# Performance work log

Measured on AMD Instinct MI355X. Metric: run time of the kernel, lower is better.

## Reference

```python
import jax, jax.numpy as jnp
import numpy as np

COMMA_ID = 1010   # BERT wordpiece id for ','
H, NH, HD = 768, 8, 96
B, S = 64, 512
NSEG = 17         # 16 commas per row -> 17 segments
EPS = 1e-5


def setup_inputs() -> dict:
    key = jax.random.key(0)
    ks = jax.random.split(key, 16)
    text_hs = jax.random.normal(ks[0], (B, S, H), jnp.float32)
    cols_hs = jax.random.normal(ks[1], (B, S, H), jnp.float32)
    ids = jax.random.randint(ks[2], (B, S), 0, 30522)
    ids = jnp.where(ids == COMMA_ID, COMMA_ID + 1, ids)  # avoid accidental commas
    comma_pos = jnp.arange(16, 257, 16)                  # 16 commas per row
    ids = ids.at[:, comma_pos].set(COMMA_ID)
    sc = 0.02
    wq = jax.random.normal(ks[3], (H, H), jnp.float32) * sc
    wk = jax.random.normal(ks[4], (H, H), jnp.float32) * sc
    wv = jax.random.normal(ks[5], (H, H), jnp.float32) * sc
    bq = jnp.zeros((H,), jnp.float32)
    bk = jnp.zeros((H,), jnp.float32)
    bv = jnp.zeros((H,), jnp.float32)
    wo = jax.random.normal(ks[6], (H, H), jnp.float32) * sc
    bo = jnp.zeros((H,), jnp.float32)
    gamma = jnp.ones((H,), jnp.float32)
    beta = jnp.zeros((H,), jnp.float32)
    w_out = jax.random.normal(ks[7], (1, H), jnp.float32) * sc
    b_out = jnp.zeros((1,), jnp.float32)
    return dict(text_hs=text_hs, cols_hs=cols_hs, wq=wq, wk=wk, wv=wv,
                bq=bq, bk=bk, bv=bv, wo=wo, bo=bo, gamma=gamma, beta=beta,
                w_out=w_out, b_out=b_out, columns_input_ids=ids, n_segments=NSEG)


def _forward(text_hs, cols_hs, wq, wk, wv, bq, bk, bv, wo, bo,
             gamma, beta, w_out, b_out, columns_input_ids, n_segments):
    t = text_hs[:, 1:, :]   # drop first token, as in forward()  [B, L, H]
    c = cols_hs[:, 1:, :]
    L = t.shape[1]
    # --- nn.MultiheadAttention(query=cols, key=value=text), batch_first ---
    q = c @ wq.T + bq
    k = t @ wk.T + bk
    v = t @ wv.T + bv
    split = lambda x: x.reshape(x.shape[0], -1, NH, HD).transpose(0, 2, 1, 3)
    scores = jnp.einsum('bhqd,bhkd->bhqk', split(q), split(k)) / np.sqrt(HD).astype(np.float32)
    attn = jax.nn.softmax(scores, axis=-1)
    ctx = jnp.einsum('bhqk,bhkd->bhqd', attn, split(v))
    ctx = ctx.transpose(0, 2, 1, 3).reshape(c.shape[0], L, H)
    attn_out = ctx @ wo.T + bo
    # --- BatchNorm1d over channels (training-mode batch stats) ---
    xt = attn_out.transpose(0, 2, 1)            # [B, H, L]
    mu = xt.mean(axis=(0, 2), keepdims=True)
    var = xt.var(axis=(0, 2), keepdims=True)     # biased, as torch BN normalization
    xn = (xt - mu) / jnp.sqrt(var + EPS) * gamma[None, :, None] + beta[None, :, None]
    cross_out = c + xn.transpose(0, 2, 1)       # residual add
    fv = (cross_out @ w_out.T + b_out).squeeze(-1)   # [B, L] scores per token
    # --- compose_outputs: mean-pool comma-delimited ragged spans ---
    is_comma = columns_input_ids[:, :L] == COMMA_ID
    seg = jnp.cumsum(is_comma.astype(jnp.int32), axis=1) - is_comma.astype(jnp.int32)
    mask = (jnp.arange(L)[None, :] >= 1) & (~is_comma)    # slice_start=1, commas excluded
    oh = ((seg[:, :, None] == jnp.arange(n_segments)[None, None, :])
          & mask[:, :, None]).astype(fv.dtype)            # [B, L, J]
    sums = jnp.einsum('blj,bl->bj', oh, fv)
    cnt = oh.sum(axis=1)
    return sums / jnp.maximum(cnt, 1.0)                   # [B, n_segments]


def reference(text_hs, cols_hs, wq, wk, wv, bq, bk, bv, wo, bo,
              gamma, beta, w_out, b_out, columns_input_ids, n_segments):
    return _forward(text_hs, cols_hs, wq, wk, wv, bq, bk, bv, wo, bo,
                    gamma, beta, w_out, b_out, columns_input_ids, n_segments)
```

## Files before the change

kernel.cpp:

```cpp
#include <hip/hip_runtime.h>
#include <hip/hip_bf16.h>

#define COMMA_IDC 1010
#define NHEAD 8
#define Ll 511
#define Mrows 32704
#define NSEG 17

typedef __attribute__((ext_vector_type(8))) short bf16x8;
typedef __attribute__((ext_vector_type(4))) float f32x4;
typedef unsigned short u16;
typedef unsigned int u32;
typedef unsigned long long u64;

__device__ __forceinline__ u16 f2b(float f) {
  __hip_bfloat16 h = __float2bfloat16(f);
  return *reinterpret_cast<u16*>(&h);
}
__device__ __forceinline__ float b2f(u16 u) {
  u32 x = ((u32)u) << 16;
  return __builtin_bit_cast(float, x);
}

__device__ __forceinline__ void gld_lds16(const void* g, void* l) {
  __builtin_amdgcn_global_load_lds(
      (const __attribute__((address_space(1))) void*)(u64)g,
      (__attribute__((address_space(3))) void*)(u32)(u64)l,
      16, 0, 0);
}

#define MFMA16(a, b, c) __builtin_amdgcn_mfma_f32_16x16x32_bf16(a, b, c, 0, 0, 0)

__global__ void conv_sliced(const float4* __restrict__ src, ushort4* __restrict__ dst) {
  int b = blockIdx.y;
  int idx = blockIdx.x * 256 + threadIdx.x;
  if (idx >= Ll * 192) return;
  int l = idx / 192, c = idx - l * 192;
  float4 v = src[(b * 512 + l + 1) * 192 + c];
  ushort4 o; o.x = f2b(v.x); o.y = f2b(v.y); o.z = f2b(v.z); o.w = f2b(v.w);
  dst[(b * Ll + l) * 192 + c] = o;
}

__global__ void conv_flat(const float4* __restrict__ src, ushort4* __restrict__ dst, int n4) {
  int i = blockIdx.x * 256 + threadIdx.x;
  if (i < n4) {
    float4 v = src[i];
    ushort4 o; o.x = f2b(v.x); o.y = f2b(v.y); o.z = f2b(v.z); o.w = f2b(v.w);
    dst[i] = o;
  }
}

__global__ void zero_kernel(float* p, int n) {
  int i = blockIdx.x * 256 + threadIdx.x;
  if (i < n) p[i] = 0.f;
}

template<int NTILES, int NOUT, int QNT>
__global__ __launch_bounds__(256) void gemmk(
    const u16* __restrict__ A0, const u16* __restrict__ A1, const u16* __restrict__ W,
    const float* __restrict__ b0, const float* __restrict__ b1, const float* __restrict__ b2,
    u16* __restrict__ outp)
{
  __shared__ __align__(16) u16 sMem[16384];
  u16* sA = sMem;
  u16* sW = sMem + 8192;

  const int tid = threadIdx.x;
  const int lane = tid & 63, wid = tid >> 6;
  int fid = blockIdx.x;
  int xcd = fid & 7, t = fid >> 3;
  int mrow = xcd * 32 + t / NTILES;
  int ncol = t - (t / NTILES) * NTILES;
  const int m0 = mrow * 128, n0 = ncol * 128;
  const u16* __restrict__ A = (ncol < QNT) ? A0 : A1;
  const int fr = lane & 15, fq = lane >> 4;
  const int wr = wid >> 1, wc = wid & 1;

  f32x4 acc[4][4] = {};

  const int r0 = tid >> 2, kc0 = tid & 3;
  const u16* gA0 = A + (u64)(m0 + r0) * 768 + kc0 * 8;
  const u16* gA1 = A + (u64)(m0 + r0 + 64) * 768 + kc0 * 8;
  const u16* gW0 = W + (u64)(n0 + r0) * 768 + kc0 * 8;
  const u16* gW1 = W + (u64)(n0 + r0 + 64) * 768 + kc0 * 8;
  u16* lA0 = sA + wid * 512;
  u16* lA1 = sA + 2048 + wid * 512;
  u16* lW0 = sW + wid * 512;
  u16* lW1 = sW + 2048 + wid * 512;

  auto STAGE = [&](int buf, int kofs) {
    gld_lds16(gA0 + kofs, lA0 + buf * 4096);
    gld_lds16(gA1 + kofs, lA1 + buf * 4096);
    gld_lds16(gW0 + kofs, lW0 + buf * 4096);
    gld_lds16(gW1 + kofs, lW1 + buf * 4096);
  };
  auto COMPUTE = [&](int buf) {
    const u16* pa = sA + buf * 4096 + (wr * 64 + fr) * 32 + fq * 8;
    const u16* pb = sW + buf * 4096 + (wc * 64 + fr) * 32 + fq * 8;
    bf16x8 a[4], b[4];
#pragma unroll
    for (int i = 0; i < 4; i++) a[i] = *(const bf16x8*)(pa + i * 16 * 32);
#pragma unroll
    for (int j = 0; j < 4; j++) b[j] = *(const bf16x8*)(pb + j * 16 * 32);
#pragma unroll
    for (int i = 0; i < 4; i++)
#pragma unroll
      for (int j = 0; j < 4; j++)
        acc[i][j] = MFMA16(a[i], b[j], acc[i][j]);
  };

  STAGE(0, 0);
  for (int k0 = 0; k0 < 768; k0 += 64) {
    __syncthreads();
    if (k0 + 32 < 768) STAGE(1, k0 + 32);
    COMPUTE(0);
    __syncthreads();
    if (k0 + 64 < 768) STAGE(0, k0 + 64);
    COMPUTE(1);
  }

  const int seg = n0 / 768, boff = n0 - seg * 768;
  const float* bp = (seg == 0) ? b0 : ((seg == 1) ? b1 : b2);
  float bj[4];
#pragma unroll
  for (int j = 0; j < 4; j++) bj[j] = bp[boff + wc * 64 + j * 16 + fr];

#pragma unroll
  for (int half = 0; half < 2; half++) {
    __syncthreads();
#pragma unroll
    for (int i2 = 0; i2 < 2; i2++) {
      int i = half * 2 + i2;
#pragma unroll
      for (int j = 0; j < 4; j++) {
#pragma unroll
        for (int r = 0; r < 4; r++) {
          int lr = wr * 32 + i2 * 16 + fq * 4 + r;
          sMem[lr * 136 + wc * 64 + j * 16 + fr] = f2b(acc[i][j][r] + bj[j]);
        }
      }
    }
    __syncthreads();
#pragma unroll
    for (int c = 0; c < 4; c++) {
      int cc = tid + c * 256;
      int lr = cc >> 4, ch = cc & 15;
      int m = m0 + (lr >> 5) * 64 + half * 32 + (lr & 31);
      if (m < Mrows)
        *(bf16x8*)(outp + (u64)m * NOUT + n0 + ch * 8) =
            *(const bf16x8*)(sMem + lr * 136 + ch * 8);
    }
  }
}

__global__ __launch_bounds__(256) void vtrans(const u16* __restrict__ QKV, u16* __restrict__ VT) {
  __shared__ __align__(16) u16 sT[128 * 128];
  int bh = blockIdx.y;
  int b = bh >> 3, h = bh & 7;
  int l0 = blockIdx.x * 128;
  u16* outp = VT + (u64)bh * 96 * 512;
  int t = threadIdx.x;
#pragma unroll
  for (int k = 0; k < 6; k++) {
    int c = t + k * 256;
    int l = c / 12, ch = c - l * 12;
    int lc = l0 + l; if (lc > 510) lc = 510;
    bf16x8 v = *(const bf16x8*)(QKV + (u64)(b * 511 + lc) * 2304 + 1536 + h * 96 + ch * 8);
    int chunk = l * 16 + (ch ^ ((l >> 3) & 7));
    *(bf16x8*)(sT + chunk * 8) = v;
  }
  __syncthreads();
#pragma unroll
  for (int k = 0; k < 6; k++) {
    int c = t + k * 256;
    int d = c >> 4, lch = c & 15;
    u16 vals[8];
#pragma unroll
    for (int k2 = 0; k2 < 8; k2++) {
      int r = lch * 8 + k2;
      int idx = r * 128 + (((d >> 3) ^ (lch & 7)) << 3) + (d & 7);
      vals[k2] = sT[idx];
    }
    bf16x8 o;
#pragma unroll
    for (int k2 = 0; k2 < 8; k2++) o[k2] = (short)vals[k2];
    *(bf16x8*)(outp + (u64)d * 512 + l0 + lch * 8) = o;
  }
}

#define PST 36
__global__ __launch_bounds__(256) void attn_kernel(
    const u16* __restrict__ QKV, const u16* __restrict__ VT, u16* __restrict__ ctxb)
{
  __shared__ __align__(16) u16 sK[32 * 96];
  __shared__ __align__(16) u16 sV[32 * 96];
  __shared__ __align__(16) u16 sP[4][16 * PST];
  const int tid = threadIdx.x, lane = tid & 63, wid = tid >> 6;
  int fid = blockIdx.x;
  int xcd = fid & 7, slot = (fid >> 3) & 3, grp = fid >> 5;
  int bh = grp * 8 + xcd;
  int b = bh >> 3, h = bh & 7;
  int q0 = slot * 128;
  const int fr = lane & 15, fq = lane >> 4;
  const u64 mb = (u64)(b * 511);
  const u64 hbV = (u64)bh * 96 * 512;

  bf16x8 qf[2][3];
#pragma unroll
  for (int sub = 0; sub < 2; sub++) {
    int qr = q0 + wid * 32 + sub * 16 + fr; if (qr > 510) qr = 510;
#pragma unroll
    for (int ks = 0; ks < 3; ks++)
      qf[sub][ks] = *(const bf16x8*)(QKV + (mb + qr) * 2304 + h * 96 + ks * 32 + fq * 8);
  }

  f32x4 ctx[2][6] = {};
  f32x4 sumP[2] = {};

  int cK1 = wid * 64 + lane;
  int kr1 = cK1 / 12, kc1 = cK1 - kr1 * 12;
  const u16* gK1 = QKV + (mb + kr1) * 2304 + 768 + h * 96 + kc1 * 8;
  int cK2 = 256 + cK1;
  int kr2 = cK2 / 12, kc2 = cK2 - kr2 * 12;
  const u16* gK2 = QKV + (mb + kr2) * 2304 + 768 + h * 96 + kc2 * 8;
  int cV1 = wid * 64 + lane;
  int dV1 = cV1 >> 2, jV1 = (cV1 & 3) ^ ((dV1 >> 1) & 3);
  const u16* gV1 = VT + hbV + (u64)dV1 * 512 + jV1 * 8;
  int cV2 = 256 + (wid - 2) * 64 + lane;
  int dV2 = cV2 >> 2, jV2 = (cV2 & 3) ^ ((dV2 >> 1) & 3);
  const u16* gV2 = VT + hbV + (u64)dV2 * 512 + jV2 * 8;

  u16* lK1 = sK + (u32)(wid * 64) * 8;
  u16* lK2 = sK + (u32)(256 + wid * 64) * 8;
  u16* lV1 = sV + (u32)(wid * 64) * 8;
  u16* lV2 = sV + (u32)(256 + (wid - 2) * 64) * 8;
  u16* pw = &sP[wid][0];

  const float cs = 0.10206207261596575f;
  const int cpx = fq ^ ((fr >> 1) & 3);

  for (int kv0 = 0; kv0 < 511; kv0 += 32) {
    __syncthreads();
    gld_lds16(gK1, lK1); gK1 += (u64)32 * 2304;
    if (wid < 2) { gld_lds16(gK2, lK2); gK2 += (u64)32 * 2304; }
    gld_lds16(gV1, lV1); gV1 += 32;
    if (wid >= 2) { gld_lds16(gV2, lV2); gV2 += 32; }
    __syncthreads();

    bf16x8 kf0[3], kf1[3];
#pragma unroll
    for (int ks = 0; ks < 3; ks++) {
      kf0[ks] = *(const bf16x8*)(sK + fr * 96 + ks * 32 + fq * 8);
      kf1[ks] = *(const bf16x8*)(sK + (16 + fr) * 96 + ks * 32 + fq * 8);
    }
    const bool ok1 = (kv0 + 16 + fr) < Ll;

#pragma unroll
    for (int sub = 0; sub < 2; sub++) {
      f32x4 s0 = {}, s1 = {};
#pragma unroll
      for (int ks = 0; ks < 3; ks++) {
        s0 = MFMA16(qf[sub][ks], kf0[ks], s0);
        s1 = MFMA16(qf[sub][ks], kf1[ks], s1);
      }
      float p0[4], p1[4];
#pragma unroll
      for (int r = 0; r < 4; r++) {
        p0[r] = __expf(s0[r] * cs);
        float e1 = __expf(s1[r] * cs);
        p1[r] = ok1 ? e1 : 0.f;
        sumP[sub][r] += p0[r] + p1[r];
      }
#pragma unroll
      for (int r = 0; r < 4; r++) {
        int row = fq * 4 + r;
        pw[row * PST + fr] = f2b(p0[r]);
        pw[row * PST + 16 + fr] = f2b(p1[r]);
      }
      bf16x8 pf = *(const bf16x8*)(pw + fr * PST + fq * 8);
#pragma unroll
      for (int df = 0; df < 6; df++) {
        bf16x8 vf = *(const bf16x8*)(sV + (df * 16 + fr) * 32 + cpx * 8);
        ctx[sub][df] = MFMA16(pf, vf, ctx[sub][df]);
      }
    }
  }

#pragma unroll
  for (int sub = 0; sub < 2; sub++) {
    float inv[4];
#pragma unroll
    for (int r = 0; r < 4; r++) {
      float s = sumP[sub][r];
      s += __shfl_xor(s, 1, 64);
      s += __shfl_xor(s, 2, 64);
      s += __shfl_xor(s, 4, 64);
      s += __shfl_xor(s, 8, 64);
      inv[r] = 1.f / s;
    }
#pragma unroll
    for (int df = 0; df < 6; df++) {
#pragma unroll
      for (int r = 0; r < 4; r++) {
        int q = q0 + wid * 32 + sub * 16 + fq * 4 + r;
        if (q < Ll)
          ctxb[(u64)(b * Ll + q) * 768 + h * 96 + df * 16 + fr] = f2b(ctx[sub][df][r] * inv[r]);
      }
    }
  }
}

__global__ __launch_bounds__(256) void stats_kernel(const u16* __restrict__ ao,
                                                    float* __restrict__ ssum, float* __restrict__ ssq)
{
  int t = threadIdx.x;
  int row0 = blockIdx.x * 128;
  int rowEnd = row0 + 128; if (rowEnd > Mrows) rowEnd = Mrows;
  float s[3] = {0.f, 0.f, 0.f}, q[3] = {0.f, 0.f, 0.f};
  for (int m = row0; m < rowEnd; m++) {
    const u16* rp = ao + (u64)m * 768;
#pragma unroll
    for (int i = 0; i < 3; i++) {
      float v = b2f(rp[t + i * 256]);
      s[i] += v; q[i] += v * v;
    }
  }
#pragma unroll
  for (int i = 0; i < 3; i++) {
    atomicAdd(&ssum[t + i * 256], s[i]);
    atomicAdd(&ssq[t + i * 256], q[i]);
  }
}

__global__ __launch_bounds__(256) void derived_kernel(
    const float* __restrict__ ssum, const float* __restrict__ ssq,
    const float* __restrict__ w_out, const float* __restrict__ b_out,
    const float* __restrict__ gamma, const float* __restrict__ beta,
    float* __restrict__ weff, float* __restrict__ consts)
{
  __shared__ float red[256];
  int t = threadIdx.x;
  float acc = 0.f;
  const float invN = 1.f / 32704.f;
#pragma unroll
  for (int i = 0; i < 3; i++) {
    int hh = t + i * 256;
    float mu = ssum[hh] * invN;
    float var = ssq[hh] * invN - mu * mu;
    float rstd = 1.f / sqrtf(var + 1e-5f);
    float we = w_out[hh] * gamma[hh] * rstd;
    weff[hh] = we;
    acc += w_out[hh] * beta[hh] - we * mu;
  }
  red[t] = acc; __syncthreads();
  for (int s = 128; s > 0; s >>= 1) { if (t < s) red[t] += red[t + s]; __syncthreads(); }
  if (t == 0) consts[0] = b_out[0] + red[0];
}

__global__ __launch_bounds__(256) void fv_kernel(
    const u16* __restrict__ ao, const u16* __restrict__ cb,
    const float* __restrict__ w_out, const float* __restrict__ weff,
    const float* __restrict__ consts, float* __restrict__ fv)
{
  int lane = threadIdx.x & 63, wid = threadIdx.x >> 6;
  int m = blockIdx.x * 4 + wid;
  if (m >= Mrows) return;
  const u16* ap = ao + (u64)m * 768;
  const u16* cp = cb + (u64)m * 768;
  float acc = 0.f;
#pragma unroll
  for (int i = 0; i < 12; i++) {
    int hh = lane + i * 64;
    acc += b2f(ap[hh]) * weff[hh] + b2f(cp[hh]) * w_out[hh];
  }
#pragma unroll
  for (int off = 1; off < 64; off <<= 1) acc += __shfl_xor(acc, off, 64);
  if (lane == 0) fv[m] = acc + consts[0];
}

__global__ __launch_bounds__(64) void seg_kernel(
    const float* __restrict__ fv, const int* __restrict__ ids, float* __restrict__ out)
{
  __shared__ float ssum[NSEG];
  __shared__ int scnt[NSEG];
  int lane = threadIdx.x;
  int b = blockIdx.x;
  if (lane < NSEG) { ssum[lane] = 0.f; scnt[lane] = 0; }
  __syncthreads();
  int carry = 0;
  for (int it = 0; it < 8; it++) {
    int l = it * 64 + lane;
    bool active = l < Ll;
    int id = active ? ids[b * 512 + l] : 0;
    bool comma = active && (id == COMMA_IDC);
    u64 cmask = __ballot(comma);
    int seg = carry + __popcll(cmask & ((1ull << lane) - 1ull));
    bool valid = active && (l >= 1) && !comma;
    if (valid && seg < NSEG) {
      atomicAdd(&ssum[seg], fv[b * Ll + l]);
      atomicAdd(&scnt[seg], 1);
    }
    carry += __popcll(cmask);
  }
  __syncthreads();
  if (lane < NSEG) {
    float c = (float)scnt[lane];
    out[b * NSEG + lane] = ssum[lane] / fmaxf(c, 1.f);
  }
}

extern "C" void kernel_launch(void* const* d_in, const int* in_sizes, int n_in,
                              void* d_out, int out_size, void* d_ws, size_t ws_size,
                              hipStream_t stream)
{
  const float* text  = (const float*)d_in[0];
  const float* cols  = (const float*)d_in[1];
  const float* wq    = (const float*)d_in[2];
  const float* wk    = (const float*)d_in[3];
  const float* wvp   = (const float*)d_in[4];
  const float* bq    = (const float*)d_in[5];
  const float* bk    = (const float*)d_in[6];
  const float* bv    = (const float*)d_in[7];
  const float* wo    = (const float*)d_in[8];
  const float* bo    = (const float*)d_in[9];
  const float* gamma = (const float*)d_in[10];
  const float* beta  = (const float*)d_in[11];
  const float* w_out = (const float*)d_in[12];
  const float* b_out = (const float*)d_in[13];
  const int*   ids   = (const int*)d_in[14];
  float* out = (float*)d_out;

  char* ws = (char*)d_ws;
  u16* cb    = (u16*)(ws + 0ull);
  u16* tb    = (u16*)(ws + 50331648ull);
  u16* wqkvb = (u16*)(ws + 100663296ull);
  u16* wob   = (u16*)(ws + 104202240ull);
  u16* QKVb  = (u16*)(ws + 105381888ull);
  u16* ctxb  = (u16*)(ws + 256376832ull);
  u16* VTb   = tb;
  u16* aob   = QKVb;
  float* ssum   = (float*)(ws + 105381888ull + 50331648ull);
  float* ssq    = ssum + 768;
  float* weff   = ssum + 1536;
  float* consts = ssum + 2304;
  float* fv     = (float*)((char*)ssum + 16384ull);

  conv_sliced<<<dim3(384, 64), 256, 0, stream>>>((const float4*)cols, (ushort4*)cb);
  conv_sliced<<<dim3(384, 64), 256, 0, stream>>>((const float4*)text, (ushort4*)tb);
  conv_flat<<<576, 256, 0, stream>>>((const float4*)wq, (ushort4*)wqkvb, 147456);
  conv_flat<<<576, 256, 0, stream>>>((const float4*)wk, (ushort4*)(wqkvb + 589824), 147456);
  conv_flat<<<576, 256, 0, stream>>>((const float4*)wvp, (ushort4*)(wqkvb + 1179648), 147456);
  conv_flat<<<576, 256, 0, stream>>>((const float4*)wo, (ushort4*)wob, 147456);

  gemmk<18, 2304, 6><<<4608, 256, 0, stream>>>(cb, tb, wqkvb, bq, bk, bv, QKVb);
  vtrans<<<dim3(4, 512), 256, 0, stream>>>(QKVb, VTb);
  attn_kernel<<<2048, 256, 0, stream>>>(QKVb, VTb, ctxb);

  zero_kernel<<<6, 256, 0, stream>>>(ssum, 1536);
  gemmk<6, 768, 99><<<1536, 256, 0, stream>>>(ctxb, ctxb, wob, bo, bo, bo, aob);
  stats_kernel<<<256, 256, 0, stream>>>(aob, ssum, ssq);
  derived_kernel<<<1, 256, 0, stream>>>(ssum, ssq, w_out, b_out, gamma, beta, weff, consts);
  fv_kernel<<<8176, 256, 0, stream>>>(aob, cb, w_out, weff, consts, fv);
  seg_kernel<<<64, 64, 0, stream>>>(fv, ids, out);
}
```

Before: 462.3 us.

## Replace 128x128 GEMM with 256x256 8-wave tiled GEMM and merge conversion launches

```diff
diff --git a/kernel.cpp b/kernel.cpp
--- a/kernel.cpp
+++ b/kernel.cpp
@@ -31,7 +31,10 @@
 
 #define MFMA16(a, b, c) __builtin_amdgcn_mfma_f32_16x16x32_bf16(a, b, c, 0, 0, 0)
 
-__global__ void conv_sliced(const float4* __restrict__ src, ushort4* __restrict__ dst) {
+__global__ void conv_sliced2(const float4* __restrict__ s0, const float4* __restrict__ s1,
+                             ushort4* __restrict__ d0, ushort4* __restrict__ d1) {
+  const float4* src = blockIdx.z ? s1 : s0;
+  ushort4* dst = blockIdx.z ? d1 : d0;
   int b = blockIdx.y;
   int idx = blockIdx.x * 256 + threadIdx.x;
   if (idx >= Ll * 192) return;
@@ -41,13 +44,16 @@
   dst[(b * Ll + l) * 192 + c] = o;
 }
 
-__global__ void conv_flat(const float4* __restrict__ src, ushort4* __restrict__ dst, int n4) {
+__global__ void conv_w(const float4* __restrict__ wq, const float4* __restrict__ wk,
+                       const float4* __restrict__ wv, const float4* __restrict__ wo,
+                       ushort4* __restrict__ wqkvb, ushort4* __restrict__ wob) {
   int i = blockIdx.x * 256 + threadIdx.x;
-  if (i < n4) {
-    float4 v = src[i];
-    ushort4 o; o.x = f2b(v.x); o.y = f2b(v.y); o.z = f2b(v.z); o.w = f2b(v.w);
-    dst[i] = o;
-  }
+  int seg = i / 147456, off = i - seg * 147456;
+  const float4* s = (seg == 0) ? wq : ((seg == 1) ? wk : ((seg == 2) ? wv : wo));
+  ushort4* d = (seg == 3) ? wob : (wqkvb + seg * 147456);
+  float4 v = s[off];
+  ushort4 o; o.x = f2b(v.x); o.y = f2b(v.y); o.z = f2b(v.z); o.w = f2b(v.w);
+  d[off] = o;
 }
 
 __global__ void zero_kernel(float* p, int n) {
@@ -55,100 +61,156 @@
   if (i < n) p[i] = 0.f;
 }
 
+#define LDA_(i, kk) (*(const bf16x8*)(sMem + bA + ((i) * 16 + fr) * 64 + ((((kk) * 4 + fq) ^ xm) << 3)))
+#define LDW_(j, kk) (*(const bf16x8*)(sMem + bW + (((wc * 64 + (j) * 16) >> 7) * 8192) + \
+                     (((wc * 64 + (j) * 16) & 127) + fr) * 64 + ((((kk) * 4 + fq) ^ xm) << 3)))
+#define LGKM0 do { asm volatile("s_waitcnt lgkmcnt(0)" ::: "memory"); __builtin_amdgcn_sched_barrier(0); } while (0)
+
 template<int NTILES, int NOUT, int QNT>
-__global__ __launch_bounds__(256) void gemmk(
+__global__ __launch_bounds__(512, 2) void gemm256(
     const u16* __restrict__ A0, const u16* __restrict__ A1, const u16* __restrict__ W,
     const float* __restrict__ b0, const float* __restrict__ b1, const float* __restrict__ b2,
     u16* __restrict__ outp)
 {
-  __shared__ __align__(16) u16 sMem[16384];
-  u16* sA = sMem;
-  u16* sW = sMem + 8192;
-
+  __shared__ __align__(16) u16 sMem[65536];
   const int tid = threadIdx.x;
   const int lane = tid & 63, wid = tid >> 6;
+  const int fr = lane & 15, fq = lane >> 4;
+  const int wr = wid >> 2, wc = wid & 3;
+  const int xm = fr & 7;
+
   int fid = blockIdx.x;
-  int xcd = fid & 7, t = fid >> 3;
-  int mrow = xcd * 32 + t / NTILES;
-  int ncol = t - (t / NTILES) * NTILES;
-  const int m0 = mrow * 128, n0 = ncol * 128;
+  int xcd = fid & 7, w = fid >> 3;
+  int mrow = xcd * 16 + w / NTILES;
+  int ncol = w - (w / NTILES) * NTILES;
+  const int m0 = mrow * 256, n0 = ncol * 256;
   const u16* __restrict__ A = (ncol < QNT) ? A0 : A1;
-  const int fr = lane & 15, fq = lane >> 4;
-  const int wr = wid >> 1, wc = wid & 1;
-
-  f32x4 acc[4][4] = {};
-
-  const int r0 = tid >> 2, kc0 = tid & 3;
-  const u16* gA0 = A + (u64)(m0 + r0) * 768 + kc0 * 8;
-  const u16* gA1 = A + (u64)(m0 + r0 + 64) * 768 + kc0 * 8;
-  const u16* gW0 = W + (u64)(n0 + r0) * 768 + kc0 * 8;
-  const u16* gW1 = W + (u64)(n0 + r0 + 64) * 768 + kc0 * 8;
-  u16* lA0 = sA + wid * 512;
-  u16* lA1 = sA + 2048 + wid * 512;
-  u16* lW0 = sW + wid * 512;
-  u16* lW1 = sW + 2048 + wid * 512;
-
-  auto STAGE = [&](int buf, int kofs) {
-    gld_lds16(gA0 + kofs, lA0 + buf * 4096);
-    gld_lds16(gA1 + kofs, lA1 + buf * 4096);
-    gld_lds16(gW0 + kofs, lW0 + buf * 4096);
-    gld_lds16(gW1 + kofs, lW1 + buf * 4096);
+
+  const int rS = tid >> 3;
+  const int cS = (tid & 7) ^ (rS & 7);
+  const u16* gA0 = A + (u64)(m0 + rS) * 768 + cS * 8;
+  const u16* gA1 = A + (u64)(m0 + 128 + rS) * 768 + cS * 8;
+  const u16* gW0 = W + (u64)(n0 + rS) * 768 + cS * 8;
+  const u16* gW1 = W + (u64)(n0 + 128 + rS) * 768 + cS * 8;
+  const u32 st0 = tid * 8;
+
+  f32x4 acc[8][4] = {};
+
+  auto stage_all = [&](int buf, int kt) {
+    const int kb = kt * 64;
+    const u32 db = (u32)buf * 32768;
+    gld_lds16(gA0 + kb, sMem + db + st0);
+    gld_lds16(gA0 + kb + 49152, sMem + db + st0 + 4096);
+    gld_lds16(gA1 + kb, sMem + db + 8192 + st0);
+    gld_lds16(gA1 + kb + 49152, sMem + db + 8192 + st0 + 4096);
+    gld_lds16(gW0 + kb, sMem + db + 16384 + st0);
+    gld_lds16(gW0 + kb + 49152, sMem + db + 16384 + st0 + 4096);
+    gld_lds16(gW1 + kb, sMem + db + 24576 + st0);
+    gld_lds16(gW1 + kb + 49152, sMem + db + 24576 + st0 + 4096);
   };
-  auto COMPUTE = [&](int buf) {
-    const u16* pa = sA + buf * 4096 + (wr * 64 + fr) * 32 + fq * 8;
-    const u16* pb = sW + buf * 4096 + (wc * 64 + fr) * 32 + fq * 8;
-    bf16x8 a[4], b[4];
-#pragma unroll
-    for (int i = 0; i < 4; i++) a[i] = *(const bf16x8*)(pa + i * 16 * 32);
-#pragma unroll
-    for (int j = 0; j < 4; j++) b[j] = *(const bf16x8*)(pb + j * 16 * 32);
+
+  stage_all(0, 0);
+  asm volatile("s_waitcnt vmcnt(0)" ::: "memory");
+  __builtin_amdgcn_s_barrier();
+
+  for (int kt = 0; kt < 12; ++kt) {
+    const u32 db = (u32)(kt & 1) * 32768;
+    const u32 bA = db + wr * 8192;
+    const u32 bW = db + 16384;
+    bf16x8 af[4][2], wf[2][2];
+
+#pragma unroll
+    for (int i = 0; i < 4; i++) { af[i][0] = LDA_(i, 0); af[i][1] = LDA_(i, 1); }
+#pragma unroll
+    for (int j = 0; j < 2; j++) { wf[j][0] = LDW_(j, 0); wf[j][1] = LDW_(j, 1); }
+    __builtin_amdgcn_s_barrier();
+    if (kt + 1 < 12) stage_all((kt + 1) & 1, kt + 1);
+    LGKM0;
+    __builtin_amdgcn_s_setprio(1);
 #pragma unroll
     for (int i = 0; i < 4; i++)
 #pragma unroll
-      for (int j = 0; j < 4; j++)
-        acc[i][j] = MFMA16(a[i], b[j], acc[i][j]);
-  };
-
-  STAGE(0, 0);
-  for (int k0 = 0; k0 < 768; k0 += 64) {
+      for (int j = 0; j < 2; j++) {
+        acc[i][j] = MFMA16(af[i][0], wf[j][0], acc[i][j]);
+        acc[i][j] = MFMA16(af[i][1], wf[j][1], acc[i][j]);
+      }
+    __builtin_amdgcn_s_setprio(0);
+    __builtin_amdgcn_s_barrier();
+
+#pragma unroll
+    for (int j = 0; j < 2; j++) { wf[j][0] = LDW_(j + 2, 0); wf[j][1] = LDW_(j + 2, 1); }
+    __builtin_amdgcn_s_barrier();
+    LGKM0;
+    __builtin_amdgcn_s_setprio(1);
+#pragma unroll
+    for (int i = 0; i < 4; i++)
+#pragma unroll
+      for (int j = 0; j < 2; j++) {
+        acc[i][j + 2] = MFMA16(af[i][0], wf[j][0], acc[i][j + 2]);
+        acc[i][j + 2] = MFMA16(af[i][1], wf[j][1], acc[i][j + 2]);
+      }
+    __builtin_amdgcn_s_setprio(0);
+    __builtin_amdgcn_s_barrier();
+
+#pragma unroll
+    for (int i = 0; i < 4; i++) { af[i][0] = LDA_(i + 4, 0); af[i][1] = LDA_(i + 4, 1); }
+#pragma unroll
+    for (int j = 0; j < 2; j++) { wf[j][0] = LDW_(j, 0); wf[j][1] = LDW_(j, 1); }
+    __builtin_amdgcn_s_barrier();
+    LGKM0;
+    __builtin_amdgcn_s_setprio(1);
+#pragma unroll
+    for (int i = 0; i < 4; i++)
+#pragma unroll
+      for (int j = 0; j < 2; j++) {
+        acc[i + 4][j] = MFMA16(af[i][0], wf[j][0], acc[i + 4][j]);
+        acc[i + 4][j] = MFMA16(af[i][1], wf[j][1], acc[i + 4][j]);
+      }
+    __builtin_amdgcn_s_setprio(0);
+    __builtin_amdgcn_s_barrier();
+
+#pragma unroll
+    for (int j = 0; j < 2; j++) { wf[j][0] = LDW_(j + 2, 0); wf[j][1] = LDW_(j + 2, 1); }
+    __builtin_amdgcn_s_barrier();
+    LGKM0;
+    __builtin_amdgcn_s_setprio(1);
+#pragma unroll
+    for (int i = 0; i < 4; i++)
+#pragma unroll
+      for (int j = 0; j < 2; j++) {
+        acc[i + 4][j + 2] = MFMA16(af[i][0], wf[j][0], acc[i + 4][j + 2]);
+        acc[i + 4][j + 2] = MFMA16(af[i][1], wf[j][1], acc[i + 4][j + 2]);
+      }
+    __builtin_amdgcn_s_setprio(0);
+    asm volatile("s_waitcnt vmcnt(0)" ::: "memory");
+    __builtin_amdgcn_s_barrier();
+  }
+
+  const float* bp = (n0 < 768) ? b0 : ((n0 < 1536) ? b1 : b2);
+  const int bcol = n0 & 767;
+  float bj[4];
+#pragma unroll
+  for (int j = 0; j < 4; j++) bj[j] = bp[bcol + wc * 64 + j * 16 + fr];
+
+#pragma unroll
+  for (int h = 0; h < 2; h++) {
     __syncthreads();
-    if (k0 + 32 < 768) STAGE(1, k0 + 32);
-    COMPUTE(0);
+    if (wr == h) {
+#pragma unroll
+      for (int i = 0; i < 8; i++)
+#pragma unroll
+        for (int j = 0; j < 4; j++)
+#pragma unroll
+          for (int r = 0; r < 4; r++)
+            sMem[(i * 16 + fq * 4 + r) * 264 + wc * 64 + j * 16 + fr] = f2b(acc[i][j][r] + bj[j]);
+    }
     __syncthreads();
-    if (k0 + 64 < 768) STAGE(0, k0 + 64);
-    COMPUTE(1);
-  }
-
-  const int seg = n0 / 768, boff = n0 - seg * 768;
-  const float* bp = (seg == 0) ? b0 : ((seg == 1) ? b1 : b2);
-  float bj[4];
-#pragma unroll
-  for (int j = 0; j < 4; j++) bj[j] = bp[boff + wc * 64 + j * 16 + fr];
-
-#pragma unroll
-  for (int half = 0; half < 2; half++) {
-    __syncthreads();
-#pragma unroll
-    for (int i2 = 0; i2 < 2; i2++) {
-      int i = half * 2 + i2;
-#pragma unroll
-      for (int j = 0; j < 4; j++) {
-#pragma unroll
-        for (int r = 0; r < 4; r++) {
-          int lr = wr * 32 + i2 * 16 + fq * 4 + r;
-          sMem[lr * 136 + wc * 64 + j * 16 + fr] = f2b(acc[i][j][r] + bj[j]);
-        }
-      }
-    }
-    __syncthreads();
-#pragma unroll
-    for (int c = 0; c < 4; c++) {
-      int cc = tid + c * 256;
-      int lr = cc >> 4, ch = cc & 15;
-      int m = m0 + (lr >> 5) * 64 + half * 32 + (lr & 31);
-      if (m < Mrows)
-        *(bf16x8*)(outp + (u64)m * NOUT + n0 + ch * 8) =
-            *(const bf16x8*)(sMem + lr * 136 + ch * 8);
+#pragma unroll
+    for (int it = 0; it < 8; it++) {
+      int chunk = tid + it * 512;
+      int lr = chunk >> 5, ch = chunk & 31;
+      *(bf16x8*)(outp + (u64)(m0 + h * 128 + lr) * NOUT + n0 + ch * 8) =
+          *(const bf16x8*)(sMem + lr * 264 + ch * 8);
     }
   }
 }
@@ -445,19 +507,18 @@
   float* consts = ssum + 2304;
   float* fv     = (float*)((char*)ssum + 16384ull);
 
-  conv_sliced<<<dim3(384, 64), 256, 0, stream>>>((const float4*)cols, (ushort4*)cb);
-  conv_sliced<<<dim3(384, 64), 256, 0, stream>>>((const float4*)text, (ushort4*)tb);
-  conv_flat<<<576, 256, 0, stream>>>((const float4*)wq, (ushort4*)wqkvb, 147456);
-  conv_flat<<<576, 256, 0, stream>>>((const float4*)wk, (ushort4*)(wqkvb + 589824), 147456);
-  conv_flat<<<576, 256, 0, stream>>>((const float4*)wvp, (ushort4*)(wqkvb + 1179648), 147456);
-  conv_flat<<<576, 256, 0, stream>>>((const float4*)wo, (ushort4*)wob, 147456);
-
-  gemmk<18, 2304, 6><<<4608, 256, 0, stream>>>(cb, tb, wqkvb, bq, bk, bv, QKVb);
+  conv_sliced2<<<dim3(384, 64, 2), 256, 0, stream>>>(
+      (const float4*)cols, (const float4*)text, (ushort4*)cb, (ushort4*)tb);
+  conv_w<<<2304, 256, 0, stream>>>(
+      (const float4*)wq, (const float4*)wk, (const float4*)wvp, (const float4*)wo,
+      (ushort4*)wqkvb, (ushort4*)wob);
+
+  gemm256<9, 2304, 3><<<1152, 512, 0, stream>>>(cb, tb, wqkvb, bq, bk, bv, QKVb);
   vtrans<<<dim3(4, 512), 256, 0, stream>>>(QKVb, VTb);
   attn_kernel<<<2048, 256, 0, stream>>>(QKVb, VTb, ctxb);
 
   zero_kernel<<<6, 256, 0, stream>>>(ssum, 1536);
-  gemmk<6, 768, 99><<<1536, 256, 0, stream>>>(ctxb, ctxb, wob, bo, bo, bo, aob);
+  gemm256<3, 768, 99><<<384, 512, 0, stream>>>(ctxb, ctxb, wob, bo, bo, bo, aob);
   stats_kernel<<<256, 256, 0, stream>>>(aob, ssum, ssq);
   derived_kernel<<<1, 256, 0, stream>>>(ssum, ssq, w_out, b_out, gamma, beta, weff, consts);
   fv_kernel<<<8176, 256, 0, stream>>>(aob, cb, w_out, weff, consts, fv);
```

Result: no change. 460.2 us (-0.5%).
